# Optimization experiments

Hardware: AMD Instinct MI355X
Metric: run time of the kernel (lower is better)

## Reference

```python
import jax, jax.numpy as jnp
import numpy as np

SPATIAL_SCALE = 0.0625
GAMMA = 0.1  # mmcv DeformRoIPool default
NUM_HEADS = 1


def deform_roi_pool(features, rois, offsets, spatial_scale=SPATIAL_SCALE, gamma=GAMMA):
    """mmcv-style deformable RoI (align) pooling, sampling_ratio=1.
    features: (B,C,H,W); rois: (N,5)=[b,x1,y1,x2,y2]; offsets: (P,oh,ow,2) (dw,dh).
    Returns (P,N,C,oh,ow)."""
    B, C, H, W = features.shape
    N = rois.shape[0]
    P, oh, ow, _ = offsets.shape
    bidx = rois[:, 0].astype(jnp.int32)
    x1 = rois[:, 1] * spatial_scale - 0.5
    y1 = rois[:, 2] * spatial_scale - 0.5
    rw = rois[:, 3] * spatial_scale - 0.5 - x1
    rh = rois[:, 4] * spatial_scale - 0.5 - y1
    bin_w = rw / ow
    bin_h = rh / oh
    gh = jnp.arange(oh, dtype=features.dtype)
    gw = jnp.arange(ow, dtype=features.dtype)
    # bin-center sample points (sampling_ratio=1), deformed by gamma*roi_size*offset
    y = (y1[:, None, None] + (gh[None, :, None] + 0.5) * bin_h[:, None, None])[None]
    y = y + gamma * rh[None, :, None, None] * offsets[:, None, :, :, 1]  # (P,N,oh,ow)
    x = (x1[:, None, None] + (gw[None, None, :] + 0.5) * bin_w[:, None, None])[None]
    x = x + gamma * rw[None, :, None, None] * offsets[:, None, :, :, 0]
    valid = (y > -1.0) & (y < H) & (x > -1.0) & (x < W)
    yc = jnp.clip(y, 0.0, H - 1)
    xc = jnp.clip(x, 0.0, W - 1)
    y0 = jnp.floor(yc).astype(jnp.int32)
    x0 = jnp.floor(xc).astype(jnp.int32)
    y1i = jnp.minimum(y0 + 1, H - 1)
    x1i = jnp.minimum(x0 + 1, W - 1)
    ly = yc - y0.astype(yc.dtype)
    lx = xc - x0.astype(xc.dtype)
    hy = 1.0 - ly
    hx = 1.0 - lx
    f = features.reshape(B, C, H * W)
    bb = jnp.broadcast_to(bidx[None, :, None, None], (P, N, oh, ow))

    def g(yi, xi):
        return f[bb, :, yi * W + xi]  # (P,N,oh,ow,C)

    val = (g(y0, x0) * (hy * hx)[..., None] + g(y0, x1i) * (hy * lx)[..., None]
           + g(y1i, x0) * (ly * hx)[..., None] + g(y1i, x1i) * (ly * lx)[..., None])
    val = jnp.where(valid[..., None], val, 0.0)
    return jnp.transpose(val, (0, 1, 4, 2, 3))  # (P,N,C,oh,ow)


def setup_inputs() -> dict:
    key = jax.random.key(0)
    ks = jax.random.split(key, 9)
    B, C, Hf, Wf = 4, 256, 128, 128
    N, oh, ow, P = 512, 7, 7, 4
    features = jax.random.normal(ks[0], (B, C, Hf, Wf), jnp.float32)
    bidx = jax.random.randint(ks[1], (N,), 0, B).astype(jnp.float32)
    xy1 = jax.random.uniform(ks[2], (N, 2), jnp.float32, 0.0, 1700.0)
    wh = jax.random.uniform(ks[3], (N, 2), jnp.float32, 32.0, 300.0)
    rois = jnp.concatenate([bidx[:, None], xy1, xy1 + wh], axis=1)  # (N,5)
    per_point_offsets = jax.random.normal(ks[4], (P, oh, ow, 2), jnp.float32) * 0.001
    queries = jax.random.normal(ks[5], (oh * ow, C), jnp.float32) * 0.02
    w_proj = jax.random.normal(ks[6], (C, C), jnp.float32) * 0.02
    b_proj = jnp.zeros((C,), jnp.float32)
    in_proj_w = jax.random.normal(ks[7], (3 * C, C), jnp.float32) * 0.02
    in_proj_b = jnp.zeros((3 * C,), jnp.float32)
    out_proj_w = jax.random.normal(ks[8], (C, C), jnp.float32) * 0.02
    out_proj_b = jnp.zeros((C,), jnp.float32)
    return dict(features=features, rois=rois, per_point_offsets=per_point_offsets,
                queries=queries, w_proj=w_proj, b_proj=b_proj,
                in_proj_w=in_proj_w, in_proj_b=in_proj_b,
                out_proj_w=out_proj_w, out_proj_b=out_proj_b)


def reference(features, rois, per_point_offsets, queries, w_proj, b_proj,
              in_proj_w, in_proj_b, out_proj_w, out_proj_b):
    samples = deform_roi_pool(features, rois, per_point_offsets)  # (P,N,C,oh,ow)
    P, N, C, oh, ow = samples.shape
    # 1x1 conv projection
    proj = jnp.einsum('pnchw,dc->pndhw', samples, w_proj) + b_proj[None, None, :, None, None]
    kv = jnp.transpose(proj, (0, 1, 3, 4, 2)).reshape(P, N * oh * ow, C)  # (P,B,C)
    q = jnp.tile(queries, (N, 1))  # (B,C), B=(n,h,w) order
    Wq, Wk, Wv = in_proj_w[:C], in_proj_w[C:2 * C], in_proj_w[2 * C:]
    bq, bk, bv = in_proj_b[:C], in_proj_b[C:2 * C], in_proj_b[2 * C:]
    H = NUM_HEADS
    d = C // H
    Q = (q @ Wq.T + bq).reshape(-1, H, d)
    K = (kv @ Wk.T + bk).reshape(P, -1, H, d)
    V = (kv @ Wv.T + bv).reshape(P, -1, H, d)
    scores = jnp.einsum('bhd,pbhd->bhp', Q, K) * (d ** -0.5)
    attn = jax.nn.softmax(scores, axis=-1)  # over the P sampled points
    out = jnp.einsum('bhp,pbhd->bhd', attn, V).reshape(-1, C)
    out = out @ out_proj_w.T + out_proj_b
    return out.reshape(N, oh, ow, C).transpose(0, 3, 1, 2)  # (N,C,oh,ow)
```

## Files before the change

### kernel.cpp

```cpp
#include <hip/hip_runtime.h>
#include <hip/hip_cooperative_groups.h>
#include <math.h>

namespace cg = cooperative_groups;

#define C_DIM 256
#define H_DIM 128
#define W_DIM 128
#define HW (H_DIM*W_DIM)
#define N_ROIS 512
#define TOKENS (N_ROIS*49)
#define SPS 0.0625f
#define GAMMA 0.1f
#define SCALE 0.0625f

typedef __attribute__((ext_vector_type(8))) short bf16x8;
typedef __attribute__((ext_vector_type(4))) float f32x4;
typedef __attribute__((ext_vector_type(8))) unsigned short us8;

__device__ inline unsigned short f2bf_rne(float f) {
    unsigned int b = __float_as_uint(f);
    b += 0x7fffu + ((b >> 16) & 1u);
    return (unsigned short)(b >> 16);
}
__device__ inline float bfu(unsigned short u) {
    return __uint_as_float(((unsigned int)u) << 16);
}


__device__ inline void dev_pre1(int idx,
                                const float* w_proj, const float* in_proj_w,
                                const float* in_proj_b, const float* queries,
                                const float* b_proj,
                                float* A_k, float* A_v, float* Qhat, float* cv) {
    if (idx < 65536) {
        int i = idx >> 8, j = idx & 255;
        const float* wk = in_proj_w + (size_t)(256 + i) * 256;
        float s = 0.f;
        for (int t = 0; t < 256; t++) s += wk[t] * w_proj[t * 256 + j];
        A_k[idx] = s;
    } else if (idx < 131072) {
        int e = idx - 65536;
        int i = e >> 8, j = e & 255;
        const float* wv = in_proj_w + (size_t)(512 + i) * 256;
        float s = 0.f;
        for (int t = 0; t < 256; t++) s += wv[t] * w_proj[t * 256 + j];
        A_v[e] = s;
    } else if (idx < 143616) {
        int e = idx - 131072;
        int s_ = e >> 8, i = e & 255;
        const float* q  = queries + (size_t)s_ * 256;
        const float* wq = in_proj_w + (size_t)i * 256;
        float s = in_proj_b[i];
        for (int t = 0; t < 256; t++) s += q[t] * wq[t];
        Qhat[e] = s;
    } else if (idx < 143872) {
        int i = idx - 143616;
        const float* wv = in_proj_w + (size_t)(512 + i) * 256;
        float s = in_proj_b[512 + i];
        for (int t = 0; t < 256; t++) s += wv[t] * b_proj[t];
        cv[i] = s;
    }
}

__device__ inline void dev_pre2(int idx,
                                const float* Qhat, const float* A_k, const float* A_v,
                                const float* out_proj_w, const float* out_proj_b,
                                const float* cv,
                                float* u, unsigned short* Mh, unsigned short* Ml,
                                float* c_out) {
    if (idx < 12544) {
        int s_ = idx >> 8, j = idx & 255;
        const float* qh = Qhat + (size_t)s_ * 256;
        float s = 0.f;
        for (int i = 0; i < 256; i++) s += qh[i] * A_k[i * 256 + j];
        u[idx] = s;
    } else if (idx < 78080) {
        int e = idx - 12544;
        int c = e >> 8, d = e & 255;
        const float* wo = out_proj_w + (size_t)c * 256;
        float s = 0.f;
        for (int i = 0; i < 256; i++) s += wo[i] * A_v[i * 256 + d];
        unsigned short hi = f2bf_rne(s);
        unsigned short lo = f2bf_rne(s - bfu(hi));
        Mh[(size_t)c * 256 + d] = hi;
        Ml[(size_t)c * 256 + d] = lo;
    } else if (idx < 78336) {
        int c = idx - 78080;
        const float* wo = out_proj_w + (size_t)c * 256;
        float s = out_proj_b[c];
        for (int i = 0; i < 256; i++) s += wo[i] * cv[i];
        c_out[c] = s;
    }
}

__device__ inline void dev_transpose_tile(char* ldsraw, int tile_id, int tid,
                                          const float* features,
                                          unsigned short* feat_b) {
    float (*tile)[65] = (float (*)[65])ldsraw;
    int b   = tile_id >> 10;
    int rem = tile_id & 1023;
    int c0  = (rem >> 8) << 6;
    int s0  = (rem & 255) << 6;
    int sl = tid & 63, cw = tid >> 6;
    const float* fin = features + (size_t)b * C_DIM * HW;
    #pragma unroll
    for (int kk = 0; kk < 16; kk++) {
        int cl = cw + kk * 4;
        tile[cl][sl] = fin[(size_t)(c0 + cl) * HW + s0 + sl];
    }
    __syncthreads();
    unsigned short* fo = feat_b + (size_t)b * HW * C_DIM;
    #pragma unroll
    for (int kk = 0; kk < 16; kk++) {
        int sl2 = cw + kk * 4;
        fo[(size_t)(s0 + sl2) * C_DIM + c0 + sl] = f2bf_rne(tile[sl][sl2]);
    }
    __syncthreads();
}

__device__ inline void dev_sample_gemm(char* ldsraw, int n, int tid,
                                       const unsigned short* feat_b,
                                       const float* rois, const float* offs,
                                       const float* u,
                                       const unsigned short* Mh,
                                       const unsigned short* Ml,
                                       const float* c_out, float* out) {
    unsigned short* A = (unsigned short*)ldsraw;

    const float* r = rois + (size_t)n * 5;
    int bi    = (int)r[0];
    float x1  = r[1] * SPS - 0.5f;
    float y1v = r[2] * SPS - 0.5f;
    float rw  = r[3] * SPS - 0.5f - x1;
    float rh  = r[4] * SPS - 0.5f - y1v;
    float bw  = rw * (1.0f / 7.0f);
    float bh  = rh * (1.0f / 7.0f);
    const unsigned short* fb = feat_b + (size_t)bi * HW * C_DIM;

    int lane32 = tid & 31;
    int halfw  = tid >> 5;
    int c8 = lane32 * 8;

    for (int t = halfw; t < 49; t += 8) {
        int hb = t / 7, wb = t - hb * 7;
        const float* up = u + (size_t)t * 256 + c8;
        float uu[8];
        *(float4*)uu       = *(const float4*)up;
        *(float4*)(uu + 4) = *(const float4*)(up + 4);

        float sv[4][8];
        float part[4];
        #pragma unroll
        for (int p = 0; p < 4; p++) {
            float offw = offs[((p * 7 + hb) * 7 + wb) * 2 + 0];
            float offh = offs[((p * 7 + hb) * 7 + wb) * 2 + 1];
            float y = y1v + ((float)hb + 0.5f) * bh + GAMMA * rh * offh;
            float x = x1  + ((float)wb + 0.5f) * bw + GAMMA * rw * offw;
            bool valid = (y > -1.0f) && (y < 128.0f) && (x > -1.0f) && (x < 128.0f);
            float yc = fminf(fmaxf(y, 0.f), 127.f);
            float xc = fminf(fmaxf(x, 0.f), 127.f);
            int y0i = (int)yc, x0i = (int)xc;
            int y1i = min(y0i + 1, 127), x1i = min(x0i + 1, 127);
            float ly = yc - (float)y0i, lx = xc - (float)x0i;
            float hy = 1.f - ly, hx = 1.f - lx;
            float w00 = hy * hx, w01 = hy * lx, w10 = ly * hx, w11 = ly * lx;
            if (!valid) { w00 = 0.f; w01 = 0.f; w10 = 0.f; w11 = 0.f; }
            us8 r00 = *(const us8*)(fb + (size_t)(y0i * W_DIM + x0i) * 256 + c8);
            us8 r01 = *(const us8*)(fb + (size_t)(y0i * W_DIM + x1i) * 256 + c8);
            us8 r10 = *(const us8*)(fb + (size_t)(y1i * W_DIM + x0i) * 256 + c8);
            us8 r11 = *(const us8*)(fb + (size_t)(y1i * W_DIM + x1i) * 256 + c8);
            float accp = 0.f;
            #pragma unroll
            for (int j = 0; j < 8; j++) {
                float v = w00 * bfu(r00[j]) + w01 * bfu(r01[j])
                        + w10 * bfu(r10[j]) + w11 * bfu(r11[j]);
                sv[p][j] = v;
                accp = fmaf(uu[j], v, accp);
            }
            part[p] = accp;
        }
        #pragma unroll
        for (int mk = 1; mk <= 16; mk <<= 1) {
            #pragma unroll
            for (int p = 0; p < 4; p++) part[p] += __shfl_xor(part[p], mk, 64);
        }
        float sc0 = part[0] * SCALE, sc1 = part[1] * SCALE;
        float sc2 = part[2] * SCALE, sc3 = part[3] * SCALE;
        float mx = fmaxf(fmaxf(sc0, sc1), fmaxf(sc2, sc3));
        float e0 = __expf(sc0 - mx), e1 = __expf(sc1 - mx);
        float e2 = __expf(sc2 - mx), e3 = __expf(sc3 - mx);
        float inv = 1.f / (e0 + e1 + e2 + e3);
        us8 o8;
        #pragma unroll
        for (int j = 0; j < 8; j++) {
            float mv = (e0 * sv[0][j] + e1 * sv[1][j]
                      + e2 * sv[2][j] + e3 * sv[3][j]) * inv;
            o8[j] = f2bf_rne(mv);
        }
        *(us8*)(A + t * 264 + c8) = o8;
    }
    for (int i = tid; i < 480; i += 256) {
        int row = 49 + (i >> 5);
        int cs = (i & 31) * 8;
        us8 z = {0, 0, 0, 0, 0, 0, 0, 0};
        *(us8*)(A + row * 264 + cs) = z;
    }
    __syncthreads();

    int lane = tid & 63;
    int wave = tid >> 6;
    int col  = lane & 15;
    int quad = lane >> 4;
    int cbase = wave * 64;

    f32x4 zero = {0.f, 0.f, 0.f, 0.f};
    f32x4 acc[4][4];
    #pragma unroll
    for (int i = 0; i < 4; i++)
        #pragma unroll
        for (int j = 0; j < 4; j++) acc[i][j] = zero;

    for (int ks = 0; ks < 8; ks++) {
        bf16x8 af[4];
        #pragma unroll
        for (int rt = 0; rt < 4; rt++)
            af[rt] = *(const bf16x8*)(A + (rt * 16 + col) * 264 + ks * 32 + quad * 8);
        #pragma unroll
        for (int ct = 0; ct < 4; ct++) {
            size_t bo = (size_t)(cbase + ct * 16 + col) * 256 + ks * 32 + quad * 8;
            bf16x8 bh8 = *(const bf16x8*)(Mh + bo);
            bf16x8 bl8 = *(const bf16x8*)(Ml + bo);
            #pragma unroll
            for (int rt = 0; rt < 4; rt++) {
                acc[rt][ct] = __builtin_amdgcn_mfma_f32_16x16x32_bf16(af[rt], bh8, acc[rt][ct], 0, 0, 0);
                acc[rt][ct] = __builtin_amdgcn_mfma_f32_16x16x32_bf16(af[rt], bl8, acc[rt][ct], 0, 0, 0);
            }
        }
    }

    __syncthreads();
    float* ostage = (float*)ldsraw;
    #pragma unroll
    for (int rt = 0; rt < 4; rt++) {
        #pragma unroll
        for (int ct = 0; ct < 4; ct++) {
            int c = cbase + ct * 16 + col;
            float bias = c_out[c];
            #pragma unroll
            for (int rr = 0; rr < 4; rr++) {
                int tt = rt * 16 + quad * 4 + rr;
                if (tt < 49) ostage[c * 53 + tt] = acc[rt][ct][rr] + bias;
            }
        }
    }
    __syncthreads();
    float* ob = out + (size_t)n * 12544;
    for (int k = 0; k < 49; k++) {
        int flat = k * 256 + tid;
        int c2 = flat / 49;
        int t2 = flat - c2 * 49;
        ob[flat] = ostage[c2 * 53 + t2];
    }
}

struct MegaArgs {
    const float* features; const float* rois; const float* offs;
    const float* queries;  const float* w_proj; const float* b_proj;
    const float* in_proj_w; const float* in_proj_b;
    const float* out_proj_w; const float* out_proj_b;
    float* A_k; float* A_v; float* Qhat; float* cv;
    float* u;   float* c_out;
    unsigned short* Mh; unsigned short* Ml;
    unsigned short* feat_b;
    float* out;
};

__global__ void __launch_bounds__(256, 2) mega(MegaArgs a) {
    __shared__ __align__(16) char ldsraw[54272];
    cg::grid_group grid = cg::this_grid();
    int tid = threadIdx.x;
    int bid = blockIdx.x;

    for (int idx = bid * 256 + tid; idx < 143872; idx += 131072)
        dev_pre1(idx, a.w_proj, a.in_proj_w, a.in_proj_b, a.queries, a.b_proj,
                 a.A_k, a.A_v, a.Qhat, a.cv);

    for (int k = 0; k < 8; k++)
        dev_transpose_tile(ldsraw, bid * 8 + k, tid, a.features, a.feat_b);

    __threadfence();
    grid.sync();
    __threadfence();

    dev_pre2(bid * 256 + tid, a.Qhat, a.A_k, a.A_v, a.out_proj_w, a.out_proj_b,
             a.cv, a.u, a.Mh, a.Ml, a.c_out);

    __threadfence();
    grid.sync();
    __threadfence();

    dev_sample_gemm(ldsraw, bid, tid, a.feat_b, a.rois, a.offs, a.u,
                    a.Mh, a.Ml, a.c_out, a.out);
}

__global__ void k_pre1(const float* w_proj, const float* in_proj_w,
                       const float* in_proj_b, const float* queries,
                       const float* b_proj,
                       float* A_k, float* A_v, float* Qhat, float* cv) {
    dev_pre1(blockIdx.x * 256 + threadIdx.x, w_proj, in_proj_w, in_proj_b,
             queries, b_proj, A_k, A_v, Qhat, cv);
}
__global__ void k_pre2(const float* Qhat, const float* A_k, const float* A_v,
                       const float* out_proj_w, const float* out_proj_b,
                       const float* cv, float* u,
                       unsigned short* Mh, unsigned short* Ml, float* c_out) {
    dev_pre2(blockIdx.x * 256 + threadIdx.x, Qhat, A_k, A_v, out_proj_w,
             out_proj_b, cv, u, Mh, Ml, c_out);
}
__global__ void k_transpose(const float* features, unsigned short* feat_b) {
    __shared__ __align__(16) char ldsraw[16640];
    dev_transpose_tile(ldsraw, blockIdx.x, threadIdx.x, features, feat_b);
}
__global__ void __launch_bounds__(256) k_fused(const unsigned short* feat_b,
                                               const float* rois, const float* offs,
                                               const float* u,
                                               const unsigned short* Mh,
                                               const unsigned short* Ml,
                                               const float* c_out, float* out) {
    __shared__ __align__(16) char ldsraw[54272];
    dev_sample_gemm(ldsraw, blockIdx.x, threadIdx.x, feat_b, rois, offs, u,
                    Mh, Ml, c_out, out);
}

__global__ void sample_generic(const float* __restrict__ feat,
                               const float* __restrict__ rois,
                               const float* __restrict__ offs,
                               const float* __restrict__ u,
                               float* __restrict__ m_out) {
    __shared__ float red[4][4];
    int token = blockIdx.x;
    int n = token / 49;
    int t = token - n * 49;
    int h = t / 7;
    int w = t - h * 7;
    const float* r = rois + (size_t)n * 5;
    int bi   = (int)r[0];
    float x1 = r[1] * SPS - 0.5f;
    float y1 = r[2] * SPS - 0.5f;
    float rw = r[3] * SPS - 0.5f - x1;
    float rh = r[4] * SPS - 0.5f - y1;
    float bw = rw * (1.0f / 7.0f);
    float bh = rh * (1.0f / 7.0f);
    int c = threadIdx.x;
    const float* fb = feat + (size_t)bi * HW * C_DIM;
    float u_c = u[(size_t)t * 256 + c];
    float sv[4], part[4];
    #pragma unroll
    for (int p = 0; p < 4; p++) {
        float offw = offs[((p * 7 + h) * 7 + w) * 2 + 0];
        float offh = offs[((p * 7 + h) * 7 + w) * 2 + 1];
        float y = y1 + ((float)h + 0.5f) * bh + GAMMA * rh * offh;
        float x = x1 + ((float)w + 0.5f) * bw + GAMMA * rw * offw;
        bool valid = (y > -1.0f) && (y < (float)H_DIM) && (x > -1.0f) && (x < (float)W_DIM);
        float yc = fminf(fmaxf(y, 0.f), 127.f);
        float xc = fminf(fmaxf(x, 0.f), 127.f);
        int y0i = (int)floorf(yc);
        int x0i = (int)floorf(xc);
        int y1i = min(y0i + 1, 127);
        int x1i = min(x0i + 1, 127);
        float ly = yc - (float)y0i, lx = xc - (float)x0i;
        float hy = 1.f - ly, hx = 1.f - lx;
        float v00 = fb[(size_t)c * HW + y0i * W_DIM + x0i];
        float v01 = fb[(size_t)c * HW + y0i * W_DIM + x1i];
        float v10 = fb[(size_t)c * HW + y1i * W_DIM + x0i];
        float v11 = fb[(size_t)c * HW + y1i * W_DIM + x1i];
        float v = hy * hx * v00 + hy * lx * v01 + ly * hx * v10 + ly * lx * v11;
        v = valid ? v : 0.f;
        sv[p] = v;
        part[p] = u_c * v;
    }
    #pragma unroll
    for (int o = 32; o >= 1; o >>= 1) {
        #pragma unroll
        for (int p = 0; p < 4; p++) part[p] += __shfl_down(part[p], o, 64);
    }
    int wv = threadIdx.x >> 6, lane = threadIdx.x & 63;
    if (lane == 0) {
        red[wv][0] = part[0]; red[wv][1] = part[1];
        red[wv][2] = part[2]; red[wv][3] = part[3];
    }
    __syncthreads();
    float sc0 = (red[0][0] + red[1][0] + red[2][0] + red[3][0]) * SCALE;
    float sc1 = (red[0][1] + red[1][1] + red[2][1] + red[3][1]) * SCALE;
    float sc2 = (red[0][2] + red[1][2] + red[2][2] + red[3][2]) * SCALE;
    float sc3 = (red[0][3] + red[1][3] + red[2][3] + red[3][3]) * SCALE;
    float mx = fmaxf(fmaxf(sc0, sc1), fmaxf(sc2, sc3));
    float e0 = __expf(sc0 - mx), e1 = __expf(sc1 - mx);
    float e2 = __expf(sc2 - mx), e3 = __expf(sc3 - mx);
    float inv = 1.f / (e0 + e1 + e2 + e3);
    m_out[(size_t)token * 256 + c] =
        (e0 * sv[0] + e1 * sv[1] + e2 * sv[2] + e3 * sv[3]) * inv;
}

__global__ void __launch_bounds__(256) roi_gemm_m(const float* m,
                                                  const unsigned short* __restrict__ Mh,
                                                  const unsigned short* __restrict__ Ml,
                                                  const float* __restrict__ c_out,
                                                  float* out) {
    __shared__ __align__(16) char ldsraw[54272];
    unsigned short* A = (unsigned short*)ldsraw;
    int tid = threadIdx.x;
    int n = blockIdx.x;
    const float* mb = m + (size_t)n * 12544;
    for (int i = tid; i < 3136; i += 256) {
        float4 f = *(const float4*)(mb + (size_t)i * 4);
        int t = i >> 6;
        int d = (i & 63) * 4;
        unsigned short* dst = A + t * 264 + d;
        dst[0] = f2bf_rne(f.x); dst[1] = f2bf_rne(f.y);
        dst[2] = f2bf_rne(f.z); dst[3] = f2bf_rne(f.w);
    }
    for (int i = tid; i < 480; i += 256) {
        int row = 49 + (i >> 5);
        int cs = (i & 31) * 8;
        us8 z = {0,0,0,0,0,0,0,0};
        *(us8*)(A + row * 264 + cs) = z;
    }
    __syncthreads();
    int lane = tid & 63, wave = tid >> 6;
    int col = lane & 15, quad = lane >> 4;
    int cbase = wave * 64;
    f32x4 zero = {0.f,0.f,0.f,0.f};
    f32x4 acc[4][4];
    #pragma unroll
    for (int i = 0; i < 4; i++)
        #pragma unroll
        for (int j = 0; j < 4; j++) acc[i][j] = zero;
    for (int ks = 0; ks < 8; ks++) {
        bf16x8 af[4];
        #pragma unroll
        for (int rt = 0; rt < 4; rt++)
            af[rt] = *(const bf16x8*)(A + (rt * 16 + col) * 264 + ks * 32 + quad * 8);
        #pragma unroll
        for (int ct = 0; ct < 4; ct++) {
            size_t bo = (size_t)(cbase + ct * 16 + col) * 256 + ks * 32 + quad * 8;
            bf16x8 bh8 = *(const bf16x8*)(Mh + bo);
            bf16x8 bl8 = *(const bf16x8*)(Ml + bo);
            #pragma unroll
            for (int rt = 0; rt < 4; rt++) {
                acc[rt][ct] = __builtin_amdgcn_mfma_f32_16x16x32_bf16(af[rt], bh8, acc[rt][ct], 0, 0, 0);
                acc[rt][ct] = __builtin_amdgcn_mfma_f32_16x16x32_bf16(af[rt], bl8, acc[rt][ct], 0, 0, 0);
            }
        }
    }
    __syncthreads();
    float* ostage = (float*)ldsraw;
    #pragma unroll
    for (int rt = 0; rt < 4; rt++) {
        #pragma unroll
        for (int ct = 0; ct < 4; ct++) {
            int c = cbase + ct * 16 + col;
            float bias = c_out[c];
            #pragma unroll
            for (int rr = 0; rr < 4; rr++) {
                int tt = rt * 16 + quad * 4 + rr;
                if (tt < 49) ostage[c * 53 + tt] = acc[rt][ct][rr] + bias;
            }
        }
    }
    __syncthreads();
    float* ob = out + (size_t)n * 12544;
    for (int k = 0; k < 49; k++) {
        int flat = k * 256 + tid;
        int c2 = flat / 49;
        int t2 = flat - c2 * 49;
        ob[flat] = ostage[c2 * 53 + t2];
    }
}

extern "C" void kernel_launch(void* const* d_in, const int* in_sizes, int n_in,
                              void* d_out, int out_size, void* d_ws, size_t ws_size,
                              hipStream_t stream) {
    (void)in_sizes; (void)n_in; (void)out_size;
    const float* features   = (const float*)d_in[0];
    const float* rois       = (const float*)d_in[1];
    const float* offs       = (const float*)d_in[2];
    const float* queries    = (const float*)d_in[3];
    const float* w_proj     = (const float*)d_in[4];
    const float* b_proj     = (const float*)d_in[5];
    const float* in_proj_w  = (const float*)d_in[6];
    const float* in_proj_b  = (const float*)d_in[7];
    const float* out_proj_w = (const float*)d_in[8];
    const float* out_proj_b = (const float*)d_in[9];
    float* out = (float*)d_out;
    float* ws  = (float*)d_ws;

    float* A_k   = ws;
    float* A_v   = A_k  + 65536;
    float* Qhat  = A_v  + 65536;
    float* cv    = Qhat + 12544;
    float* u     = cv   + 256;
    float* c_out = u    + 12544;
    unsigned short* Mh = (unsigned short*)(ws + 156672);
    unsigned short* Ml = (unsigned short*)(ws + 189440);
    unsigned short* feat_b = (unsigned short*)(ws + 222208);
    float* m_fb = ws + 222208;

    size_t needT = ((size_t)222208 + (size_t)8388608) * 4;
    size_t needF = ((size_t)222208 + (size_t)TOKENS * 256) * 4;
    bool useT = ws_size >= needT;

    if (useT) {
        int nb = 0;
        hipError_t oe = hipOccupancyMaxActiveBlocksPerMultiprocessor(&nb, mega, 256, 0);
        bool coop = (oe == hipSuccess) && (nb >= 2);

        if (coop) {
            MegaArgs ha;
            ha.features = features; ha.rois = rois; ha.offs = offs; ha.queries = queries;
            ha.w_proj = w_proj; ha.b_proj = b_proj; ha.in_proj_w = in_proj_w;
            ha.in_proj_b = in_proj_b; ha.out_proj_w = out_proj_w; ha.out_proj_b = out_proj_b;
            ha.A_k = A_k; ha.A_v = A_v; ha.Qhat = Qhat; ha.cv = cv;
            ha.u = u; ha.c_out = c_out; ha.Mh = Mh; ha.Ml = Ml;
            ha.feat_b = feat_b; ha.out = out;
            void* kp[] = { &ha };
            hipError_t le = hipLaunchCooperativeKernel(
                reinterpret_cast<void*>(mega), dim3(N_ROIS), dim3(256), kp, 0, stream);
            if (le == hipSuccess) return;
            (void)hipGetLastError();
        }
        k_pre1<<<562, 256, 0, stream>>>(w_proj, in_proj_w, in_proj_b, queries,
                                        b_proj, A_k, A_v, Qhat, cv);
        k_transpose<<<4096, 256, 0, stream>>>(features, feat_b);
        k_pre2<<<306, 256, 0, stream>>>(Qhat, A_k, A_v, out_proj_w, out_proj_b,
                                        cv, u, Mh, Ml, c_out);
        k_fused<<<N_ROIS, 256, 0, stream>>>(feat_b, rois, offs, u, Mh, Ml, c_out, out);
    } else {
        k_pre1<<<562, 256, 0, stream>>>(w_proj, in_proj_w, in_proj_b, queries,
                                        b_proj, A_k, A_v, Qhat, cv);
        k_pre2<<<306, 256, 0, stream>>>(Qhat, A_k, A_v, out_proj_w, out_proj_b,
                                        cv, u, Mh, Ml, c_out);
        float* m = (ws_size >= needF) ? m_fb : out;
        sample_generic<<<TOKENS, 256, 0, stream>>>(features, rois, offs, u, m);
        roi_gemm_m<<<N_ROIS, 256, 0, stream>>>(m, Mh, Ml, c_out, out);
    }
}
```

Before: 222.5 us.

## Replace cooperative megakernel with three stream-ordered kernels and fused init

Drops the cooperative launch and its two grid-wide barriers. The work now runs as three ordinary launches: a merged init kernel that does the feature transpose to bf16 plus the first weight precompute in one grid, then the second precompute, then the fused sample-and-GEMM kernel. The aim is to avoid grid.sync overhead and the two-blocks-per-CU occupancy cap of the megakernel, and to let the transpose spread over many more blocks. The cost is extra launch boundaries between stages. Pointers also gain __restrict__ qualifiers.

```diff
diff --git a/kernel.cpp b/kernel.cpp
--- a/kernel.cpp
+++ b/kernel.cpp
@@ -1,8 +1,5 @@
 #include <hip/hip_runtime.h>
-#include <hip/hip_cooperative_groups.h>
 #include <math.h>
-
-namespace cg = cooperative_groups;
 
 #define C_DIM 256
 #define H_DIM 128
@@ -27,12 +24,14 @@
     return __uint_as_float(((unsigned int)u) << 16);
 }
 
-
-__device__ inline void dev_pre1(int idx,
-                                const float* w_proj, const float* in_proj_w,
-                                const float* in_proj_b, const float* queries,
-                                const float* b_proj,
-                                float* A_k, float* A_v, float* Qhat, float* cv) {
+__device__ inline void pre1_body(int idx,
+                                 const float* __restrict__ w_proj,
+                                 const float* __restrict__ in_proj_w,
+                                 const float* __restrict__ in_proj_b,
+                                 const float* __restrict__ queries,
+                                 const float* __restrict__ b_proj,
+                                 float* __restrict__ A_k, float* __restrict__ A_v,
+                                 float* __restrict__ Qhat, float* __restrict__ cv) {
     if (idx < 65536) {
         int i = idx >> 8, j = idx & 255;
         const float* wk = in_proj_w + (size_t)(256 + i) * 256;
@@ -63,12 +62,63 @@
     }
 }
 
-__device__ inline void dev_pre2(int idx,
-                                const float* Qhat, const float* A_k, const float* A_v,
-                                const float* out_proj_w, const float* out_proj_b,
-                                const float* cv,
-                                float* u, unsigned short* Mh, unsigned short* Ml,
-                                float* c_out) {
+__global__ void __launch_bounds__(256) k_init(
+        const float* __restrict__ features, unsigned short* __restrict__ feat_b,
+        const float* __restrict__ w_proj, const float* __restrict__ in_proj_w,
+        const float* __restrict__ in_proj_b, const float* __restrict__ queries,
+        const float* __restrict__ b_proj,
+        float* __restrict__ A_k, float* __restrict__ A_v,
+        float* __restrict__ Qhat, float* __restrict__ cv) {
+    int tid = threadIdx.x;
+    int bid = blockIdx.x;
+    if (bid < 4096) {
+        __shared__ float tile[64][65];
+        int b   = bid >> 10;
+        int rem = bid & 1023;
+        int c0  = (rem >> 8) << 6;
+        int s0  = (rem & 255) << 6;
+        int sl = tid & 63, cw = tid >> 6;
+        const float* fin = features + (size_t)b * C_DIM * HW;
+        #pragma unroll
+        for (int kk = 0; kk < 16; kk++) {
+            int cl = cw + kk * 4;
+            tile[cl][sl] = fin[(size_t)(c0 + cl) * HW + s0 + sl];
+        }
+        __syncthreads();
+        unsigned short* fo = feat_b + (size_t)b * HW * C_DIM;
+        #pragma unroll
+        for (int kk = 0; kk < 16; kk++) {
+            int sl2 = cw + kk * 4;
+            fo[(size_t)(s0 + sl2) * C_DIM + c0 + sl] = f2bf_rne(tile[sl][sl2]);
+        }
+    } else {
+        pre1_body((bid - 4096) * 256 + tid, w_proj, in_proj_w, in_proj_b,
+                  queries, b_proj, A_k, A_v, Qhat, cv);
+    }
+}
+
+__global__ void k_pre1(const float* __restrict__ w_proj,
+                       const float* __restrict__ in_proj_w,
+                       const float* __restrict__ in_proj_b,
+                       const float* __restrict__ queries,
+                       const float* __restrict__ b_proj,
+                       float* __restrict__ A_k, float* __restrict__ A_v,
+                       float* __restrict__ Qhat, float* __restrict__ cv) {
+    pre1_body(blockIdx.x * 256 + threadIdx.x, w_proj, in_proj_w, in_proj_b,
+              queries, b_proj, A_k, A_v, Qhat, cv);
+}
+
+__global__ void k_pre2(const float* __restrict__ Qhat,
+                       const float* __restrict__ A_k,
+                       const float* __restrict__ A_v,
+                       const float* __restrict__ out_proj_w,
+                       const float* __restrict__ out_proj_b,
+                       const float* __restrict__ cv,
+                       float* __restrict__ u,
+                       unsigned short* __restrict__ Mh,
+                       unsigned short* __restrict__ Ml,
+                       float* __restrict__ c_out) {
+    int idx = blockIdx.x * 256 + threadIdx.x;
     if (idx < 12544) {
         int s_ = idx >> 8, j = idx & 255;
         const float* qh = Qhat + (size_t)s_ * 256;
@@ -94,39 +144,20 @@
     }
 }
 
-__device__ inline void dev_transpose_tile(char* ldsraw, int tile_id, int tid,
-                                          const float* features,
-                                          unsigned short* feat_b) {
-    float (*tile)[65] = (float (*)[65])ldsraw;
-    int b   = tile_id >> 10;
-    int rem = tile_id & 1023;
-    int c0  = (rem >> 8) << 6;
-    int s0  = (rem & 255) << 6;
-    int sl = tid & 63, cw = tid >> 6;
-    const float* fin = features + (size_t)b * C_DIM * HW;
-    #pragma unroll
-    for (int kk = 0; kk < 16; kk++) {
-        int cl = cw + kk * 4;
-        tile[cl][sl] = fin[(size_t)(c0 + cl) * HW + s0 + sl];
-    }
-    __syncthreads();
-    unsigned short* fo = feat_b + (size_t)b * HW * C_DIM;
-    #pragma unroll
-    for (int kk = 0; kk < 16; kk++) {
-        int sl2 = cw + kk * 4;
-        fo[(size_t)(s0 + sl2) * C_DIM + c0 + sl] = f2bf_rne(tile[sl][sl2]);
-    }
-    __syncthreads();
-}
-
-__device__ inline void dev_sample_gemm(char* ldsraw, int n, int tid,
-                                       const unsigned short* feat_b,
-                                       const float* rois, const float* offs,
-                                       const float* u,
-                                       const unsigned short* Mh,
-                                       const unsigned short* Ml,
-                                       const float* c_out, float* out) {
+__global__ void __launch_bounds__(256) fused_sample_gemm(
+        const unsigned short* __restrict__ feat_b,
+        const float* __restrict__ rois,
+        const float* __restrict__ offs,
+        const float* __restrict__ u,
+        const unsigned short* __restrict__ Mh,
+        const unsigned short* __restrict__ Ml,
+        const float* __restrict__ c_out,
+        float* __restrict__ out) {
+    __shared__ __align__(16) char ldsraw[54272];
     unsigned short* A = (unsigned short*)ldsraw;
+
+    int tid = threadIdx.x;
+    int n = blockIdx.x;
 
     const float* r = rois + (size_t)n * 5;
     int bi    = (int)r[0];
@@ -262,75 +293,6 @@
         int t2 = flat - c2 * 49;
         ob[flat] = ostage[c2 * 53 + t2];
     }
-}
-
-struct MegaArgs {
-    const float* features; const float* rois; const float* offs;
-    const float* queries;  const float* w_proj; const float* b_proj;
-    const float* in_proj_w; const float* in_proj_b;
-    const float* out_proj_w; const float* out_proj_b;
-    float* A_k; float* A_v; float* Qhat; float* cv;
-    float* u;   float* c_out;
-    unsigned short* Mh; unsigned short* Ml;
-    unsigned short* feat_b;
-    float* out;
-};
-
-__global__ void __launch_bounds__(256, 2) mega(MegaArgs a) {
-    __shared__ __align__(16) char ldsraw[54272];
-    cg::grid_group grid = cg::this_grid();
-    int tid = threadIdx.x;
-    int bid = blockIdx.x;
-
-    for (int idx = bid * 256 + tid; idx < 143872; idx += 131072)
-        dev_pre1(idx, a.w_proj, a.in_proj_w, a.in_proj_b, a.queries, a.b_proj,
-                 a.A_k, a.A_v, a.Qhat, a.cv);
-
-    for (int k = 0; k < 8; k++)
-        dev_transpose_tile(ldsraw, bid * 8 + k, tid, a.features, a.feat_b);
-
-    __threadfence();
-    grid.sync();
-    __threadfence();
-
-    dev_pre2(bid * 256 + tid, a.Qhat, a.A_k, a.A_v, a.out_proj_w, a.out_proj_b,
-             a.cv, a.u, a.Mh, a.Ml, a.c_out);
-
-    __threadfence();
-    grid.sync();
-    __threadfence();
-
-    dev_sample_gemm(ldsraw, bid, tid, a.feat_b, a.rois, a.offs, a.u,
-                    a.Mh, a.Ml, a.c_out, a.out);
-}
-
-__global__ void k_pre1(const float* w_proj, const float* in_proj_w,
-                       const float* in_proj_b, const float* queries,
-                       const float* b_proj,
-                       float* A_k, float* A_v, float* Qhat, float* cv) {
-    dev_pre1(blockIdx.x * 256 + threadIdx.x, w_proj, in_proj_w, in_proj_b,
-             queries, b_proj, A_k, A_v, Qhat, cv);
-}
-__global__ void k_pre2(const float* Qhat, const float* A_k, const float* A_v,
-                       const float* out_proj_w, const float* out_proj_b,
-                       const float* cv, float* u,
-                       unsigned short* Mh, unsigned short* Ml, float* c_out) {
-    dev_pre2(blockIdx.x * 256 + threadIdx.x, Qhat, A_k, A_v, out_proj_w,
-             out_proj_b, cv, u, Mh, Ml, c_out);
-}
-__global__ void k_transpose(const float* features, unsigned short* feat_b) {
-    __shared__ __align__(16) char ldsraw[16640];
-    dev_transpose_tile(ldsraw, blockIdx.x, threadIdx.x, features, feat_b);
-}
-__global__ void __launch_bounds__(256) k_fused(const unsigned short* feat_b,
-                                               const float* rois, const float* offs,
-                                               const float* u,
-                                               const unsigned short* Mh,
-                                               const unsigned short* Ml,
-                                               const float* c_out, float* out) {
-    __shared__ __align__(16) char ldsraw[54272];
-    dev_sample_gemm(ldsraw, blockIdx.x, threadIdx.x, feat_b, rois, offs, u,
-                    Mh, Ml, c_out, out);
 }
 
 __global__ void sample_generic(const float* __restrict__ feat,
@@ -403,11 +365,11 @@
         (e0 * sv[0] + e1 * sv[1] + e2 * sv[2] + e3 * sv[3]) * inv;
 }
 
-__global__ void __launch_bounds__(256) roi_gemm_m(const float* m,
+__global__ void __launch_bounds__(256) roi_gemm_m(const float* __restrict__ m,
                                                   const unsigned short* __restrict__ Mh,
                                                   const unsigned short* __restrict__ Ml,
                                                   const float* __restrict__ c_out,
-                                                  float* out) {
+                                                  float* __restrict__ out) {
     __shared__ __align__(16) char ldsraw[54272];
     unsigned short* A = (unsigned short*)ldsraw;
     int tid = threadIdx.x;
@@ -512,33 +474,17 @@
     bool useT = ws_size >= needT;
 
     if (useT) {
-        int nb = 0;
-        hipError_t oe = hipOccupancyMaxActiveBlocksPerMultiprocessor(&nb, mega, 256, 0);
-        bool coop = (oe == hipSuccess) && (nb >= 2);
-
-        if (coop) {
-            MegaArgs ha;
-            ha.features = features; ha.rois = rois; ha.offs = offs; ha.queries = queries;
-            ha.w_proj = w_proj; ha.b_proj = b_proj; ha.in_proj_w = in_proj_w;
-            ha.in_proj_b = in_proj_b; ha.out_proj_w = out_proj_w; ha.out_proj_b = out_proj_b;
-            ha.A_k = A_k; ha.A_v = A_v; ha.Qhat = Qhat; ha.cv = cv;
-            ha.u = u; ha.c_out = c_out; ha.Mh = Mh; ha.Ml = Ml;
-            ha.feat_b = feat_b; ha.out = out;
-            void* kp[] = { &ha };
-            hipError_t le = hipLaunchCooperativeKernel(
-                reinterpret_cast<void*>(mega), dim3(N_ROIS), dim3(256), kp, 0, stream);
-            if (le == hipSuccess) return;
-            (void)hipGetLastError();
-        }
-        k_pre1<<<562, 256, 0, stream>>>(w_proj, in_proj_w, in_proj_b, queries,
-                                        b_proj, A_k, A_v, Qhat, cv);
-        k_transpose<<<4096, 256, 0, stream>>>(features, feat_b);
+        k_init<<<4096 + 562, 256, 0, stream>>>(features, feat_b,
+                                               w_proj, in_proj_w, in_proj_b,
+                                               queries, b_proj,
+                                               A_k, A_v, Qhat, cv);
         k_pre2<<<306, 256, 0, stream>>>(Qhat, A_k, A_v, out_proj_w, out_proj_b,
                                         cv, u, Mh, Ml, c_out);
-        k_fused<<<N_ROIS, 256, 0, stream>>>(feat_b, rois, offs, u, Mh, Ml, c_out, out);
+        fused_sample_gemm<<<N_ROIS, 256, 0, stream>>>(feat_b, rois, offs, u,
+                                                      Mh, Ml, c_out, out);
     } else {
-        k_pre1<<<562, 256, 0, stream>>>(w_proj, in_proj_w, in_proj_b, queries,
-                                        b_proj, A_k, A_v, Qhat, cv);
+        k_pre1<<<562, 256, 0, stream>>>(w_proj, in_proj_w, in_proj_b,
+                                        queries, b_proj, A_k, A_v, Qhat, cv);
         k_pre2<<<306, 256, 0, stream>>>(Qhat, A_k, A_v, out_proj_w, out_proj_b,
                                         cv, u, Mh, Ml, c_out);
         float* m = (ws_size >= needF) ? m_fb : out;
```

New measurement: 187.0 us. -16.0%, faster.
